# Performance work log

Hardware: AMD Instinct MI355X
Metric: run time of the kernel (lower is better)

Reference implementation:

```python
import jax, jax.numpy as jnp
import numpy as np

VOCAB, INPUT, HIDDEN = 100, 512, 1024
BATCH, SEQ = 64, 512


def setup_inputs() -> dict:
    key = jax.random.key(0)
    ks = jax.random.split(key, 12)
    s = 0.02
    inp = {
        "X": jax.random.randint(ks[0], (BATCH, SEQ), 0, VOCAB, dtype=jnp.int64 if jax.config.jax_enable_x64 else jnp.int32),
        "h0": jnp.zeros((BATCH, HIDDEN), jnp.float32),
        "c0": jnp.zeros((BATCH, HIDDEN), jnp.float32),
        "emb": jax.random.normal(ks[1], (VOCAB, INPUT), jnp.float32) * s,
        "Wf_w": jax.random.normal(ks[2], (HIDDEN, INPUT + HIDDEN), jnp.float32) * s,
        "Wf_b": jnp.zeros((HIDDEN,), jnp.float32),
        "Wi_w": jax.random.normal(ks[3], (HIDDEN, INPUT + HIDDEN), jnp.float32) * s,
        "Wi_b": jnp.zeros((HIDDEN,), jnp.float32),
        "Wo_w": jax.random.normal(ks[4], (HIDDEN, INPUT + HIDDEN), jnp.float32) * s,
        "Wo_b": jnp.zeros((HIDDEN,), jnp.float32),
        "Wg_w": jax.random.normal(ks[5], (HIDDEN, INPUT + HIDDEN), jnp.float32) * s,
        "Wg_b": jnp.zeros((HIDDEN,), jnp.float32),
    }
    return inp


def reference(X, h0, c0, emb, Wf_w, Wf_b, Wi_w, Wi_b, Wo_w, Wo_b, Wg_w, Wg_b):
    # Fuse the 4 gate Linears into one GEMM (same math, concatenated rows).
    W = jnp.concatenate([Wf_w, Wi_w, Wo_w, Wg_w], axis=0)   # [4H, I+H]
    b = jnp.concatenate([Wf_b, Wi_b, Wo_b, Wg_b], axis=0)   # [4H]
    H = Wf_w.shape[0]

    xs = emb[X]                       # [B, S, I]
    xs = jnp.swapaxes(xs, 0, 1)       # [S, B, I] for scan over time

    def step(carry, x_t):
        h, c = carry
        combined = jnp.concatenate([x_t, h], axis=1)          # [B, I+H]
        z = combined @ W.T + b                                # [B, 4H]
        ft = jax.nn.sigmoid(z[:, 0*H:1*H])
        it = jax.nn.sigmoid(z[:, 1*H:2*H])
        ot = jax.nn.sigmoid(z[:, 2*H:3*H])
        gt = jnp.tanh(z[:, 3*H:4*H])
        c_t = ft * c + it * gt
        h_t = ot * jnp.tanh(c_t)
        return (h_t, c_t), h_t

    (h_f, c_f), hs = jax.lax.scan(step, (h0, c0), xs)
    latent = jnp.swapaxes(hs, 0, 1)   # [B, S, H]
    return latent, (h_f, c_f)
```

## Files before the change

kernel.cpp:

```cpp
#include <hip/hip_runtime.h>


typedef _Float16 f16x8 __attribute__((ext_vector_type(8)));
typedef float    f32x4 __attribute__((ext_vector_type(4)));
typedef unsigned int u32x4 __attribute__((ext_vector_type(4)));

#define VOCABN 100
#define SENT 0x7F7F7F7Fu

__global__ void k0_zxtable(const float* __restrict__ emb,
                           const float* __restrict__ Wf, const float* __restrict__ bf,
                           const float* __restrict__ Wi, const float* __restrict__ bi,
                           const float* __restrict__ Wo, const float* __restrict__ bo,
                           const float* __restrict__ Wg, const float* __restrict__ bg_,
                           float* __restrict__ zx) {
  const int bid = blockIdx.x;
  const int g = bid >> 6, chunk = bid & 63;
  const float* W = (g==0)?Wf:(g==1)?Wi:(g==2)?Wo:Wg;
  const float* B = (g==0)?bf:(g==1)?bi:(g==2)?bo:bg_;
  __shared__ float Wl[16][516];
  const int tid = threadIdx.x;
  for (int i = tid; i < 2048; i += 256) {
    int r = i >> 7, c4 = i & 127;
    float4 v = *(const float4*)&W[(size_t)(chunk*16 + r)*1536 + c4*4];
    Wl[r][c4*4+0]=v.x; Wl[r][c4*4+1]=v.y; Wl[r][c4*4+2]=v.z; Wl[r][c4*4+3]=v.w;
  }
  __syncthreads();
  const int u = tid & 15, vi = tid >> 4;
  for (int v0 = 0; v0 < VOCABN; v0 += 16) {
    int v = v0 + vi;
    if (v < VOCABN) {
      const float* er = emb + (size_t)v*512;
      float acc = 0.f;
      #pragma unroll 8
      for (int k = 0; k < 512; k++) acc += er[k]*Wl[u][k];
      zx[(size_t)v*4096 + g*1024 + chunk*16 + u] = acc + B[chunk*16 + u];
    }
  }
}

__global__ void k1_prep(const float* __restrict__ Wf, const float* __restrict__ Wi,
                        const float* __restrict__ Wo, const float* __restrict__ Wg,
                        _Float16* __restrict__ Whh) {
  const int bid = blockIdx.x, tid = threadIdx.x;
  #pragma unroll
  for (int i = 0; i < 4; i++) {
    int F = bid*1024 + i*256 + tid;
    int g = F >> 18;
    int rem = F & ((1<<18)-1);
    int n = rem >> 8, k4 = rem & 255;
    const float* W = (g==0)?Wf:(g==1)?Wi:(g==2)?Wo:Wg;
    float4 v = *(const float4*)&W[(size_t)n*1536 + 512 + k4*4];
    _Float16 h4[4] = {(_Float16)v.x,(_Float16)v.y,(_Float16)v.z,(_Float16)v.w};
    *(unsigned long long*)&Whh[((size_t)g<<20) + (n<<10) + (k4<<2)] =
        *(unsigned long long*)h4;
  }
}

__global__ __launch_bounds__(512, 2) void lstm_main(
    const int* __restrict__ X, const float* __restrict__ h0,
    const float* __restrict__ c0, const float* __restrict__ zx,
    const _Float16* __restrict__ Whh, float* out)
{
  const int bid = blockIdx.x;
  const int bg  = bid >> 5;
  const int js  = bid & 31;
  const int tid = threadIdx.x;
  const int w   = tid >> 6;
  const int lane = tid & 63;
  const int lm = lane & 15, lh = lane >> 4;

  __shared__ alignas(16) _Float16 hs[16][1032];
  __shared__ float zsh[8][132];

  f16x8 bw[32];
  {
    const _Float16* wp = Whh + ((size_t)(w>>1)<<20)
                       + ((size_t)(js*32 + (w&1)*16 + lm)<<10) + (lh<<3);
    #pragma unroll
    for (int kk = 0; kk < 32; kk++) bw[kk] = *(const f16x8*)(wp + kk*32);
  }

  const int sr = tid >> 6, sc = tid & 63;
  const float* h0p = h0 + (size_t)(bg*8 + sr)*1024 + sc*4;
  float* lat = out;

  const int b = (tid >> 5) & 7, u = tid & 31;
  const int brow = bg*8 + b, ucol = js*32 + u;
  float c = 0.f;
  const int* Xr = nullptr;
  if (tid < 256) {
    c = c0[(size_t)brow*1024 + ucol];
    Xr = X + (size_t)brow*512;
  }

  for (int t = 0; t < 512; t++) {
    float zx0=0.f, zx1=0.f, zx2=0.f, zx3=0.f;
    if (tid < 256) {
      int xv = Xr[t];
      const float* p = zx + (size_t)xv*4096 + ucol;
      zx0 = p[0]; zx1 = p[1024]; zx2 = p[2048]; zx3 = p[3072];
    }

    {
      const float* src = t ? (lat + ((size_t)(bg*8+sr)*512 + (t-1))*1024 + sc*4) : h0p;
      u32x4 v0, v1, v2, v3;
      for (;;) {
        asm volatile(
          "global_load_dwordx4 %0, %4, off sc1\n\t"
          "global_load_dwordx4 %1, %4, off offset:1024 sc1\n\t"
          "global_load_dwordx4 %2, %4, off offset:2048 sc1\n\t"
          "global_load_dwordx4 %3, %4, off offset:3072 sc1\n\t"
          "s_waitcnt vmcnt(0)"
          : "=&v"(v0), "=&v"(v1), "=&v"(v2), "=&v"(v3)
          : "v"(src));
        if (t == 0) break;
        bool bad = (v0.x==SENT)|(v0.y==SENT)|(v0.z==SENT)|(v0.w==SENT)
                 | (v1.x==SENT)|(v1.y==SENT)|(v1.z==SENT)|(v1.w==SENT)
                 | (v2.x==SENT)|(v2.y==SENT)|(v2.z==SENT)|(v2.w==SENT)
                 | (v3.x==SENT)|(v3.y==SENT)|(v3.z==SENT)|(v3.w==SENT);
        if (!bad) break;
        __builtin_amdgcn_s_sleep(1);
      }
      _Float16* dst = &hs[sr][sc*4];
      #define CVT_STORE(vv, J) { \
        _Float16 h4[4]; \
        h4[0]=(_Float16)__uint_as_float(vv.x); h4[1]=(_Float16)__uint_as_float(vv.y); \
        h4[2]=(_Float16)__uint_as_float(vv.z); h4[3]=(_Float16)__uint_as_float(vv.w); \
        *(unsigned long long*)(dst + J*256) = *(unsigned long long*)h4; }
      CVT_STORE(v0, 0) CVT_STORE(v1, 1) CVT_STORE(v2, 2) CVT_STORE(v3, 3)
      #undef CVT_STORE
    }
    __syncthreads();

    f32x4 a0={0,0,0,0}, a1={0,0,0,0}, a2={0,0,0,0}, a3={0,0,0,0};
    const _Float16* hrow = &hs[lm][lh<<3];
    #pragma unroll
    for (int kk = 0; kk < 32; kk += 4) {
      f16x8 x0 = *(const f16x8*)(hrow + (kk+0)*32);
      f16x8 x1 = *(const f16x8*)(hrow + (kk+1)*32);
      f16x8 x2 = *(const f16x8*)(hrow + (kk+2)*32);
      f16x8 x3 = *(const f16x8*)(hrow + (kk+3)*32);
      a0 = __builtin_amdgcn_mfma_f32_16x16x32_f16(x0, bw[kk+0], a0, 0, 0, 0);
      a1 = __builtin_amdgcn_mfma_f32_16x16x32_f16(x1, bw[kk+1], a1, 0, 0, 0);
      a2 = __builtin_amdgcn_mfma_f32_16x16x32_f16(x2, bw[kk+2], a2, 0, 0, 0);
      a3 = __builtin_amdgcn_mfma_f32_16x16x32_f16(x3, bw[kk+3], a3, 0, 0, 0);
    }
    f32x4 z4 = (a0 + a1) + (a2 + a3);
    if (lh < 2) {
      #pragma unroll
      for (int r4 = 0; r4 < 4; r4++) zsh[lh*4 + r4][w*16 + lm] = z4[r4];
    }
    __syncthreads();

    if (tid < 256) {
      float zf = zsh[b][u]      + zx0;
      float zi = zsh[b][32+u]   + zx1;
      float zo = zsh[b][64+u]   + zx2;
      float zg = zsh[b][96+u]   + zx3;
      float fg = 1.f/(1.f + expf(-zf));
      float ig = 1.f/(1.f + expf(-zi));
      float og = 1.f/(1.f + expf(-zo));
      float gg = tanhf(zg);
      c = fg*c + ig*gg;
      float h = og*tanhf(c);
      __hip_atomic_store(lat + ((size_t)brow*512 + t)*1024 + ucol, h,
                         __ATOMIC_RELAXED, __HIP_MEMORY_SCOPE_AGENT);
      if (t == 511) {
        out[33554432 + (brow<<10) + ucol] = h;
        out[33619968 + (brow<<10) + ucol] = c;
      }
    }
    __syncthreads();
  }
}

extern "C" void kernel_launch(void* const* d_in, const int* in_sizes, int n_in,
                              void* d_out, int out_size, void* d_ws, size_t ws_size,
                              hipStream_t stream) {
  const int*   X   = (const int*)  d_in[0];
  const float* h0  = (const float*)d_in[1];
  const float* c0  = (const float*)d_in[2];
  const float* emb = (const float*)d_in[3];
  const float* Wf  = (const float*)d_in[4];  const float* bf = (const float*)d_in[5];
  const float* Wi  = (const float*)d_in[6];  const float* bi = (const float*)d_in[7];
  const float* Wo  = (const float*)d_in[8];  const float* bo = (const float*)d_in[9];
  const float* Wg  = (const float*)d_in[10]; const float* bg = (const float*)d_in[11];
  float* out = (float*)d_out;

  char* ws = (char*)d_ws;
  float*    zx  = (float*)   ws;
  _Float16* Whh = (_Float16*)(ws + 1638400);

  hipMemsetAsync(out, 0x7F, (size_t)64*512*1024*4, stream);
  k0_zxtable<<<256, 256, 0, stream>>>(emb, Wf, bf, Wi, bi, Wo, bo, Wg, bg, zx);
  k1_prep<<<1024, 256, 0, stream>>>(Wf, Wi, Wo, Wg, Whh);
  lstm_main<<<256, 512, 0, stream>>>(X, h0, c0, zx, Whh, out);
}
```

Baseline: 1.603 ms.

## Replace sentinel-polling h exchange with flag-based fp16 double-buffered handoff

Drops the 128MB sentinel memset and the polling of fp32 latent rows. Each block now publishes a per-step flag after writing packed fp16 h into a double-buffered workspace, and consumers spin on 32 producer flags before loading half as many bytes. It also adds an XOR-swizzled LDS layout, fast exp-based sigmoid and tanh, and nontemporal latent stores. The risks are the relaxed-ordering flag protocol, which has no explicit release fence, and slightly lower accuracy from the approximate transcendentals.

```diff
diff --git a/kernel.cpp b/kernel.cpp
--- a/kernel.cpp
+++ b/kernel.cpp
@@ -6,7 +6,6 @@
 typedef unsigned int u32x4 __attribute__((ext_vector_type(4)));
 
 #define VOCABN 100
-#define SENT 0x7F7F7F7Fu
 
 __global__ void k0_zxtable(const float* __restrict__ emb,
                            const float* __restrict__ Wf, const float* __restrict__ bf,
@@ -60,7 +59,8 @@
 __global__ __launch_bounds__(512, 2) void lstm_main(
     const int* __restrict__ X, const float* __restrict__ h0,
     const float* __restrict__ c0, const float* __restrict__ zx,
-    const _Float16* __restrict__ Whh, float* out)
+    const _Float16* __restrict__ Whh, _Float16* __restrict__ hx,
+    int* __restrict__ flags, float* out)
 {
   const int bid = blockIdx.x;
   const int bg  = bid >> 5;
@@ -70,7 +70,7 @@
   const int lane = tid & 63;
   const int lm = lane & 15, lh = lane >> 4;
 
-  __shared__ alignas(16) _Float16 hs[16][1032];
+  __shared__ alignas(16) _Float16 hs[16*1024];
   __shared__ float zsh[8][132];
 
   f16x8 bw[32];
@@ -78,12 +78,16 @@
     const _Float16* wp = Whh + ((size_t)(w>>1)<<20)
                        + ((size_t)(js*32 + (w&1)*16 + lm)<<10) + (lh<<3);
     #pragma unroll
-    for (int kk = 0; kk < 32; kk++) bw[kk] = *(const f16x8*)(wp + kk*32);
+    for (int kk = 0; kk < 32; kk++) {
+      asm volatile("global_load_dwordx4 %0, %1, off"
+                   : "=&v"(bw[kk]) : "v"(wp + kk*32));
+    }
+    asm volatile("s_waitcnt vmcnt(0)");
+    __builtin_amdgcn_sched_barrier(0);
   }
 
   const int sr = tid >> 6, sc = tid & 63;
-  const float* h0p = h0 + (size_t)(bg*8 + sr)*1024 + sc*4;
-  float* lat = out;
+  const int fidx = (bg << 5) + (sc >> 1);
 
   const int b = (tid >> 5) & 7, u = tid & 31;
   const int brow = bg*8 + b, ucol = js*32 + u;
@@ -93,6 +97,11 @@
     c = c0[(size_t)brow*1024 + ucol];
     Xr = X + (size_t)brow*512;
   }
+  float* latp = out + (size_t)brow*512*1024 + ucol;
+
+  char* hrow_w = (char*)hs + (sr << 11);
+  const char* hrow_r = (const char*)hs + (lm << 11);
+  const int sww = (sr & 7) << 4, swr = (lm & 7) << 4;
 
   for (int t = 0; t < 512; t++) {
     float zx0=0.f, zx1=0.f, zx2=0.f, zx3=0.f;
@@ -102,45 +111,40 @@
       zx0 = p[0]; zx1 = p[1024]; zx2 = p[2048]; zx3 = p[3072];
     }
 
-    {
-      const float* src = t ? (lat + ((size_t)(bg*8+sr)*512 + (t-1))*1024 + sc*4) : h0p;
-      u32x4 v0, v1, v2, v3;
-      for (;;) {
-        asm volatile(
-          "global_load_dwordx4 %0, %4, off sc1\n\t"
-          "global_load_dwordx4 %1, %4, off offset:1024 sc1\n\t"
-          "global_load_dwordx4 %2, %4, off offset:2048 sc1\n\t"
-          "global_load_dwordx4 %3, %4, off offset:3072 sc1\n\t"
-          "s_waitcnt vmcnt(0)"
-          : "=&v"(v0), "=&v"(v1), "=&v"(v2), "=&v"(v3)
-          : "v"(src));
-        if (t == 0) break;
-        bool bad = (v0.x==SENT)|(v0.y==SENT)|(v0.z==SENT)|(v0.w==SENT)
-                 | (v1.x==SENT)|(v1.y==SENT)|(v1.z==SENT)|(v1.w==SENT)
-                 | (v2.x==SENT)|(v2.y==SENT)|(v2.z==SENT)|(v2.w==SENT)
-                 | (v3.x==SENT)|(v3.y==SENT)|(v3.z==SENT)|(v3.w==SENT);
-        if (!bad) break;
-        __builtin_amdgcn_s_sleep(1);
-      }
-      _Float16* dst = &hs[sr][sc*4];
-      #define CVT_STORE(vv, J) { \
-        _Float16 h4[4]; \
-        h4[0]=(_Float16)__uint_as_float(vv.x); h4[1]=(_Float16)__uint_as_float(vv.y); \
-        h4[2]=(_Float16)__uint_as_float(vv.z); h4[3]=(_Float16)__uint_as_float(vv.w); \
-        *(unsigned long long*)(dst + J*256) = *(unsigned long long*)h4; }
-      CVT_STORE(v0, 0) CVT_STORE(v1, 1) CVT_STORE(v2, 2) CVT_STORE(v3, 3)
-      #undef CVT_STORE
+    if (t == 0) {
+      const float* s0 = h0 + ((size_t)(bg*8+sr)<<10) + (sc<<4);
+      float4 f0 = *(const float4*)(s0+0),  f1 = *(const float4*)(s0+4);
+      float4 f2 = *(const float4*)(s0+8),  f3 = *(const float4*)(s0+12);
+      _Float16 hh[16] = {(_Float16)f0.x,(_Float16)f0.y,(_Float16)f0.z,(_Float16)f0.w,
+                         (_Float16)f1.x,(_Float16)f1.y,(_Float16)f1.z,(_Float16)f1.w,
+                         (_Float16)f2.x,(_Float16)f2.y,(_Float16)f2.z,(_Float16)f2.w,
+                         (_Float16)f3.x,(_Float16)f3.y,(_Float16)f3.z,(_Float16)f3.w};
+      int off = (sc << 5) ^ sww;
+      *(u32x4*)(hrow_w + off)        = *(u32x4*)&hh[0];
+      *(u32x4*)(hrow_w + (off ^ 16)) = *(u32x4*)&hh[8];
+    } else {
+      while (__hip_atomic_load(&flags[fidx], __ATOMIC_RELAXED,
+                               __HIP_MEMORY_SCOPE_AGENT) < t) {}
+      const _Float16* src = hx + (((t-1)&1)<<16) + ((size_t)(bg*8+sr)<<10) + (sc<<4);
+      u32x4 va, vb;
+      asm volatile(
+        "global_load_dwordx4 %0, %2, off sc1\n\t"
+        "global_load_dwordx4 %1, %2, off offset:16 sc1\n\t"
+        "s_waitcnt vmcnt(0)"
+        : "=&v"(va), "=&v"(vb) : "v"(src));
+      int off = (sc << 5) ^ sww;
+      *(u32x4*)(hrow_w + off)        = va;
+      *(u32x4*)(hrow_w + (off ^ 16)) = vb;
     }
     __syncthreads();
 
     f32x4 a0={0,0,0,0}, a1={0,0,0,0}, a2={0,0,0,0}, a3={0,0,0,0};
-    const _Float16* hrow = &hs[lm][lh<<3];
     #pragma unroll
     for (int kk = 0; kk < 32; kk += 4) {
-      f16x8 x0 = *(const f16x8*)(hrow + (kk+0)*32);
-      f16x8 x1 = *(const f16x8*)(hrow + (kk+1)*32);
-      f16x8 x2 = *(const f16x8*)(hrow + (kk+2)*32);
-      f16x8 x3 = *(const f16x8*)(hrow + (kk+3)*32);
+      f16x8 x0 = *(const f16x8*)(hrow_r + ((((kk+0)<<6) + (lh<<4)) ^ swr));
+      f16x8 x1 = *(const f16x8*)(hrow_r + ((((kk+1)<<6) + (lh<<4)) ^ swr));
+      f16x8 x2 = *(const f16x8*)(hrow_r + ((((kk+2)<<6) + (lh<<4)) ^ swr));
+      f16x8 x3 = *(const f16x8*)(hrow_r + ((((kk+3)<<6) + (lh<<4)) ^ swr));
       a0 = __builtin_amdgcn_mfma_f32_16x16x32_f16(x0, bw[kk+0], a0, 0, 0, 0);
       a1 = __builtin_amdgcn_mfma_f32_16x16x32_f16(x1, bw[kk+1], a1, 0, 0, 0);
       a2 = __builtin_amdgcn_mfma_f32_16x16x32_f16(x2, bw[kk+2], a2, 0, 0, 0);
@@ -153,25 +157,41 @@
     }
     __syncthreads();
 
+    float h = 0.f;
     if (tid < 256) {
       float zf = zsh[b][u]      + zx0;
       float zi = zsh[b][32+u]   + zx1;
       float zo = zsh[b][64+u]   + zx2;
       float zg = zsh[b][96+u]   + zx3;
-      float fg = 1.f/(1.f + expf(-zf));
-      float ig = 1.f/(1.f + expf(-zi));
-      float og = 1.f/(1.f + expf(-zo));
-      float gg = tanhf(zg);
+      float fg = 1.f/(1.f + __expf(-zf));
+      float ig = 1.f/(1.f + __expf(-zi));
+      float og = 1.f/(1.f + __expf(-zo));
+      float e2g = __expf(2.f*zg);
+      float gg = 1.f - 2.f/(e2g + 1.f);
       c = fg*c + ig*gg;
-      float h = og*tanhf(c);
-      __hip_atomic_store(lat + ((size_t)brow*512 + t)*1024 + ucol, h,
-                         __ATOMIC_RELAXED, __HIP_MEMORY_SCOPE_AGENT);
+      float e2c = __expf(2.f*c);
+      h = og*(1.f - 2.f/(e2c + 1.f));
+      if (t < 511) {
+        _Float16 hf = (_Float16)h;
+        unsigned short hu = __builtin_bit_cast(unsigned short, hf);
+        unsigned pu = (unsigned)__shfl_xor((int)hu, 1);
+        if ((u & 1) == 0) {
+          unsigned word = (unsigned)hu | (pu << 16);
+          __hip_atomic_store((unsigned*)(hx + ((t&1)<<16) + ((size_t)brow<<10) + ucol),
+                             word, __ATOMIC_RELAXED, __HIP_MEMORY_SCOPE_AGENT);
+        }
+      }
+    }
+    __syncthreads();
+    if (tid == 0 && t < 511)
+      __hip_atomic_store(&flags[bid], t+1, __ATOMIC_RELAXED, __HIP_MEMORY_SCOPE_AGENT);
+    if (tid < 256) {
+      __builtin_nontemporal_store(h, latp + (size_t)t*1024);
       if (t == 511) {
-        out[33554432 + (brow<<10) + ucol] = h;
-        out[33619968 + (brow<<10) + ucol] = c;
+        out[33554432 + ((size_t)brow<<10) + ucol] = h;
+        out[33619968 + ((size_t)brow<<10) + ucol] = c;
       }
     }
-    __syncthreads();
   }
 }
 
@@ -189,11 +209,13 @@
   float* out = (float*)d_out;
 
   char* ws = (char*)d_ws;
-  float*    zx  = (float*)   ws;
-  _Float16* Whh = (_Float16*)(ws + 1638400);
-
-  hipMemsetAsync(out, 0x7F, (size_t)64*512*1024*4, stream);
+  float*    zx    = (float*)   ws;
+  _Float16* Whh   = (_Float16*)(ws + 1638400);
+  _Float16* hx    = (_Float16*)(ws + 1638400 + 8388608);
+  int*      flags = (int*)     (ws + 1638400 + 8388608 + 262144);
+
+  hipMemsetAsync(flags, 0, 256*sizeof(int), stream);
   k0_zxtable<<<256, 256, 0, stream>>>(emb, Wf, bf, Wi, bi, Wo, bo, Wg, bg, zx);
   k1_prep<<<1024, 256, 0, stream>>>(Wf, Wi, Wo, Wg, Whh);
-  lstm_main<<<256, 512, 0, stream>>>(X, h0, c0, zx, Whh, out);
-}
+  lstm_main<<<256, 512, 0, stream>>>(X, h0, c0, zx, Whh, hx, flags, out);
+}
```

After: 1.580 ms. No clear change (-1.4%).
